# Optimization experiments

Hardware: AMD Instinct MI355X
Metric: run time of the kernel (lower is better)

Reference implementation:

```python
import jax, jax.numpy as jnp
import numpy as np

N_NODES = 5
B, C, H, W = 4, 256, 32, 32
THRESH = 0.3
EPS = 1e-12


def setup_inputs() -> dict:
    key = jax.random.key(0)
    k1, k2, k3, k4 = jax.random.split(key, 4)
    x = jax.random.normal(k1, (N_NODES, B, C, H, W), dtype=jnp.float32)
    w = jax.random.normal(k2, (N_NODES, N_NODES), dtype=jnp.float32)
    # 5 stacked conv1x1 'experts': Conv2d(2C -> C, k=1) weight [C,2C] + bias [C]
    conv_w = jax.random.normal(k3, (N_NODES, C, 2 * C), dtype=jnp.float32) * 0.02
    conv_b = jax.random.normal(k4, (N_NODES, C), dtype=jnp.float32) * 0.02
    return {"x": x, "w": w, "conv_w": conv_w, "conv_b": conv_b}


def reference(x, w, conv_w, conv_b):
    # x: [N, B, C, H, W] -- the list of N node feature maps stacked
    N, b, c, h, ww = x.shape
    P = b * c * h * ww  # 'pixels' = total element count of one node tensor

    # conv_i(cat(node_j, node_i + node_j)) splits into W1@node_j + W2@(node_i+node_j) + b_i
    W1 = conv_w[:, :, :c]          # [N, C, C] acts on node_j
    W2 = conv_w[:, :, c:]          # [N, C, C] acts on node_i + node_j
    A = W1 + W2                    # combined weight on node_j

    term_j = jnp.einsum('ick,jbkhw->ijbchw', A, x)    # [N,N,B,C,H,W]
    term_i = jnp.einsum('ick,ibkhw->ibchw', W2, x)    # [N,B,C,H,W]
    target = term_j + term_i[:, None] + conv_b[:, None, None, :, None, None]
    distance = x[None, :] - target                    # distance[i,j] = node_j - conv_i(...)

    # edge_list[:, i, j] = flatten(distance[i, j])  -> [P, N, N]
    edge = distance.reshape(N, N, P).transpose(2, 0, 1)

    # new_edge = edge * w; sigmoid; threshold at 0.3; L2-normalize over dim=2 (j axis)
    e = jax.nn.sigmoid(edge * w)
    e = jnp.where(e > THRESH, e, jnp.zeros_like(e))
    norm = jnp.sqrt(jnp.sum(e * e, axis=2, keepdims=True))
    e = e / jnp.maximum(norm, EPS)

    # node matrix: [P, N] of flattened node features; fuse h[p,i] = sum_j e[p,i,j]*node[p,j]
    node = x.reshape(N, P).T
    hmat = jnp.einsum('pij,pj->pi', e, node)          # [P, N]
    return hmat.T.reshape(N, b, c, h, ww)
```

## Files before the change

### kernel.cpp

```cpp
#include <hip/hip_runtime.h>
#include <cmath>

#define NN  5
#define BB  4
#define CCH 256
#define HWD 1024
#define THRESH_V 0.3f
#define EPS_V 1e-12f

#define CT 32
#define WT 32
#define KC 32
#define APAD 36
#define SPAD 36

#define SMEM_FLOATS 7424

__global__ __launch_bounds__(384, 4)
void fub_main(const float* __restrict__ x, const float* __restrict__ wmat,
              const float* __restrict__ conv_w, const float* __restrict__ conv_b,
              float* __restrict__ out)
{
    __shared__ __align__(16) float smem[SMEM_FLOATS];
    float* Xs  = smem;
    float* As  = smem + 5120;
    float* W2s = smem + 6272;
    float* Es  = smem;

    const int tid  = threadIdx.x;
    const int wv   = tid >> 6;
    const int lane = tid & 63;

    int bid = blockIdx.x;
    const int hwt = bid & 31; bid >>= 5;
    const int b   = bid & 3;  bid >>= 2;
    const int ct  = bid & 7;  bid >>= 3;
    const int i   = bid;

    const int c0  = ct * CT;
    const int hw0 = hwt * WT;

    const int lr = (lane >> 3) << 2;
    const int lc = (lane & 7)  << 2;

    const int jx = (wv < 5) ? wv : i;
    const float* M = (wv == 5) ? W2s : As;
    const float* Mb = M + lr;
    const float* Xb = Xs + jx * (KC * WT) + lc;

    float acc[4][4];
#pragma unroll
    for (int r = 0; r < 4; ++r)
#pragma unroll
        for (int c = 0; c < 4; ++c) acc[r][c] = 0.0f;

    for (int k0 = 0; k0 < CCH; k0 += KC) {
        if (tid < 320) {
#pragma unroll
            for (int it = 0; it < 4; ++it) {
                const int t   = tid + it * 320;
                const int j   = t >> 8;
                const int rem = t & 255;
                const int kk  = rem >> 3;
                const int p4  = (rem & 7) << 2;
                const float4 v = *(const float4*)(
                    x + (size_t)((j * BB + b) * CCH + k0 + kk) * HWD + hw0 + p4);
                *(float4*)(Xs + j * (KC * WT) + kk * WT + p4) = v;
            }
        } else {
            const int u = tid - 320;
#pragma unroll
            for (int it = 0; it < 4; ++it) {
                const int t  = u + (it << 6);
                const int r  = t >> 3;
                const int kq = (t & 7) << 2;
                const float* base =
                    conv_w + (size_t)(i * CCH + c0 + r) * (2 * CCH) + k0 + kq;
                const float4 w1 = *(const float4*)(base);
                const float4 w2 = *(const float4*)(base + CCH);
                As [(kq + 0) * APAD + r] = w1.x + w2.x;
                As [(kq + 1) * APAD + r] = w1.y + w2.y;
                As [(kq + 2) * APAD + r] = w1.z + w2.z;
                As [(kq + 3) * APAD + r] = w1.w + w2.w;
                W2s[(kq + 0) * APAD + r] = w2.x;
                W2s[(kq + 1) * APAD + r] = w2.y;
                W2s[(kq + 2) * APAD + r] = w2.z;
                W2s[(kq + 3) * APAD + r] = w2.w;
            }
        }
        __syncthreads();

#pragma unroll
        for (int kk = 0; kk < KC; ++kk) {
            const float4 a  = *(const float4*)(Mb + kk * APAD);
            const float4 xv = *(const float4*)(Xb + kk * WT);
            const float ar[4] = {a.x, a.y, a.z, a.w};
            const float xc[4] = {xv.x, xv.y, xv.z, xv.w};
#pragma unroll
            for (int r = 0; r < 4; ++r)
#pragma unroll
                for (int c = 0; c < 4; ++c)
                    acc[r][c] = fmaf(ar[r], xc[c], acc[r][c]);
        }
        __syncthreads();
    }

#pragma unroll
    for (int r = 0; r < 4; ++r) {
        *(float4*)(Es + wv * (CT * SPAD) + (lr + r) * SPAD + lc) =
            make_float4(acc[r][0], acc[r][1], acc[r][2], acc[r][3]);
    }
    __syncthreads();

    if (tid < 256) {
        const int row = tid >> 3;
        const int col = (tid & 7) << 2;
        const int c   = c0 + row;
        const float bias = conv_b[i * CCH + c];

        float wrow[NN];
#pragma unroll
        for (int j = 0; j < NN; ++j) wrow[j] = wmat[i * NN + j];

        const float4 T = *(const float4*)(Es + 5 * (CT * SPAD) + row * SPAD + col);
        const float Tv[4] = {T.x, T.y, T.z, T.w};

        float num[4] = {0.f, 0.f, 0.f, 0.f};
        float sq [4] = {0.f, 0.f, 0.f, 0.f};
#pragma unroll
        for (int j = 0; j < NN; ++j) {
            const float4 s  = *(const float4*)(Es + j * (CT * SPAD) + row * SPAD + col);
            const float4 xj = *(const float4*)(
                x + (size_t)((j * BB + b) * CCH + c) * HWD + hw0 + col);
            const float sv[4] = {s.x, s.y, s.z, s.w};
            const float xv[4] = {xj.x, xj.y, xj.z, xj.w};
#pragma unroll
            for (int cc = 0; cc < 4; ++cc) {
                const float target = sv[cc] + Tv[cc] + bias;
                const float dist   = xv[cc] - target;
                const float z      = dist * wrow[j];
                float e = 1.0f / (1.0f + expf(-z));
                e = (e > THRESH_V) ? e : 0.0f;
                sq[cc]  = fmaf(e, e, sq[cc]);
                num[cc] = fmaf(e, xv[cc], num[cc]);
            }
        }
        float res[4];
#pragma unroll
        for (int cc = 0; cc < 4; ++cc)
            res[cc] = num[cc] / fmaxf(sqrtf(sq[cc]), EPS_V);

        *(float4*)(out + (size_t)((i * BB + b) * CCH + c) * HWD + hw0 + col) =
            make_float4(res[0], res[1], res[2], res[3]);
    }
}

extern "C" void kernel_launch(void* const* d_in, const int* in_sizes, int n_in,
                              void* d_out, int out_size, void* d_ws, size_t ws_size,
                              hipStream_t stream) {
    const float* x      = (const float*)d_in[0];
    const float* w      = (const float*)d_in[1];
    const float* conv_w = (const float*)d_in[2];
    const float* conv_b = (const float*)d_in[3];
    float* out = (float*)d_out;

    dim3 grid(5120);
    dim3 block(384);
    fub_main<<<grid, block, 0, stream>>>(x, w, conv_w, conv_b, out);
}
```

Baseline: 361.5 us.

## Give each wave private LDS tiles with register prefetch and wider pixel tiles

Each wave now stages its own X slice and its own combined weight tile in a private LDS region. This removes both block-wide barriers from the K loop, and the next K chunk is prefetched into registers while the current one is computed. The pixel tile grows to 64 with 8x4 accumulators per thread, halving the grid, and the epilogue uses __expf. In exchange, weight loads are repeated by every wave, LDS use per block rises sharply, which may cut resident blocks, and register pressure grows.

```diff
diff --git a/kernel.cpp b/kernel.cpp
--- a/kernel.cpp
+++ b/kernel.cpp
@@ -9,12 +9,13 @@
 #define EPS_V 1e-12f
 
 #define CT 32
-#define WT 32
-#define KC 32
+#define WT 64
+#define KC 16
 #define APAD 36
-#define SPAD 36
+#define NCHUNK (CCH / KC)
 
-#define SMEM_FLOATS 7424
+#define ESP 68
+#define SMEM_FLOATS 13056
 
 __global__ __launch_bounds__(384, 4)
 void fub_main(const float* __restrict__ x, const float* __restrict__ wmat,
@@ -22,17 +23,13 @@
               float* __restrict__ out)
 {
     __shared__ __align__(16) float smem[SMEM_FLOATS];
-    float* Xs  = smem;
-    float* As  = smem + 5120;
-    float* W2s = smem + 6272;
-    float* Es  = smem;
 
     const int tid  = threadIdx.x;
     const int wv   = tid >> 6;
     const int lane = tid & 63;
 
     int bid = blockIdx.x;
-    const int hwt = bid & 31; bid >>= 5;
+    const int hwt = bid & 15; bid >>= 4;
     const int b   = bid & 3;  bid >>= 2;
     const int ct  = bid & 7;  bid >>= 3;
     const int i   = bid;
@@ -40,118 +37,136 @@
     const int c0  = ct * CT;
     const int hw0 = hwt * WT;
 
-    const int lr = (lane >> 3) << 2;
-    const int lc = (lane & 7)  << 2;
+    float* Xw = smem + wv * (KC * WT);
+    float* Aw = smem + 6144 + wv * (KC * APAD);
+
+    const int lr = (lane >> 4) << 3;
+    const int lc = (lane & 15) << 2;
 
     const int jx = (wv < 5) ? wv : i;
-    const float* M = (wv == 5) ? W2s : As;
-    const float* Mb = M + lr;
-    const float* Xb = Xs + jx * (KC * WT) + lc;
 
-    float acc[4][4];
+    const float* xg = x + (size_t)((jx * BB + b) * CCH) * HWD + hw0;
+    const int xk  = lane >> 4;
+    const int xc4 = (lane & 15) << 2;
+    const int acr = lane >> 1;
+    const int akq = (lane & 1) << 3;
+    const float* wg = conv_w + (size_t)(i * CCH + c0 + acr) * (2 * CCH) + akq;
+
+    float acc[8][4];
 #pragma unroll
-    for (int r = 0; r < 4; ++r)
+    for (int r = 0; r < 8; ++r)
 #pragma unroll
         for (int c = 0; c < 4; ++c) acc[r][c] = 0.0f;
 
-    for (int k0 = 0; k0 < CCH; k0 += KC) {
-        if (tid < 320) {
-#pragma unroll
-            for (int it = 0; it < 4; ++it) {
-                const int t   = tid + it * 320;
-                const int j   = t >> 8;
-                const int rem = t & 255;
-                const int kk  = rem >> 3;
-                const int p4  = (rem & 7) << 2;
-                const float4 v = *(const float4*)(
-                    x + (size_t)((j * BB + b) * CCH + k0 + kk) * HWD + hw0 + p4);
-                *(float4*)(Xs + j * (KC * WT) + kk * WT + p4) = v;
-            }
-        } else {
-            const int u = tid - 320;
-#pragma unroll
-            for (int it = 0; it < 4; ++it) {
-                const int t  = u + (it << 6);
-                const int r  = t >> 3;
-                const int kq = (t & 7) << 2;
-                const float* base =
-                    conv_w + (size_t)(i * CCH + c0 + r) * (2 * CCH) + k0 + kq;
-                const float4 w1 = *(const float4*)(base);
-                const float4 w2 = *(const float4*)(base + CCH);
-                As [(kq + 0) * APAD + r] = w1.x + w2.x;
-                As [(kq + 1) * APAD + r] = w1.y + w2.y;
-                As [(kq + 2) * APAD + r] = w1.z + w2.z;
-                As [(kq + 3) * APAD + r] = w1.w + w2.w;
-                W2s[(kq + 0) * APAD + r] = w2.x;
-                W2s[(kq + 1) * APAD + r] = w2.y;
-                W2s[(kq + 2) * APAD + r] = w2.z;
-                W2s[(kq + 3) * APAD + r] = w2.w;
-            }
-        }
-        __syncthreads();
+    float4 xr[4];
+    float4 w1a, w1b, w2a, w2b;
 
 #pragma unroll
-        for (int kk = 0; kk < KC; ++kk) {
-            const float4 a  = *(const float4*)(Mb + kk * APAD);
-            const float4 xv = *(const float4*)(Xb + kk * WT);
-            const float ar[4] = {a.x, a.y, a.z, a.w};
+    for (int it = 0; it < 4; ++it)
+        xr[it] = *(const float4*)(xg + (size_t)(xk + it * 4) * HWD + xc4);
+    w1a = *(const float4*)(wg);
+    w1b = *(const float4*)(wg + 4);
+    w2a = *(const float4*)(wg + CCH);
+    w2b = *(const float4*)(wg + CCH + 4);
+
+    for (int ch = 0; ch < NCHUNK; ++ch) {
+#pragma unroll
+        for (int it = 0; it < 4; ++it)
+            *(float4*)(Xw + (xk + it * 4) * WT + xc4) = xr[it];
+
+        float av[8];
+        if (wv != 5) {
+            av[0] = w1a.x + w2a.x; av[1] = w1a.y + w2a.y;
+            av[2] = w1a.z + w2a.z; av[3] = w1a.w + w2a.w;
+            av[4] = w1b.x + w2b.x; av[5] = w1b.y + w2b.y;
+            av[6] = w1b.z + w2b.z; av[7] = w1b.w + w2b.w;
+        } else {
+            av[0] = w2a.x; av[1] = w2a.y; av[2] = w2a.z; av[3] = w2a.w;
+            av[4] = w2b.x; av[5] = w2b.y; av[6] = w2b.z; av[7] = w2b.w;
+        }
+#pragma unroll
+        for (int t = 0; t < 8; ++t)
+            Aw[(akq + t) * APAD + acr] = av[t];
+
+        if (ch + 1 < NCHUNK) {
+            const int k0n = (ch + 1) * KC;
+#pragma unroll
+            for (int it = 0; it < 4; ++it)
+                xr[it] = *(const float4*)(xg + (size_t)(k0n + xk + it * 4) * HWD + xc4);
+            const float* wgn = wg + k0n;
+            w1a = *(const float4*)(wgn);
+            w1b = *(const float4*)(wgn + 4);
+            w2a = *(const float4*)(wgn + CCH);
+            w2b = *(const float4*)(wgn + CCH + 4);
+        }
+
+#pragma unroll
+        for (int k = 0; k < KC; ++k) {
+            const float4 a0 = *(const float4*)(Aw + k * APAD + lr);
+            const float4 a1 = *(const float4*)(Aw + k * APAD + lr + 4);
+            const float4 xv = *(const float4*)(Xw + k * WT + lc);
+            const float ar[8] = {a0.x, a0.y, a0.z, a0.w, a1.x, a1.y, a1.z, a1.w};
             const float xc[4] = {xv.x, xv.y, xv.z, xv.w};
 #pragma unroll
-            for (int r = 0; r < 4; ++r)
+            for (int r = 0; r < 8; ++r)
 #pragma unroll
                 for (int c = 0; c < 4; ++c)
                     acc[r][c] = fmaf(ar[r], xc[c], acc[r][c]);
         }
-        __syncthreads();
     }
 
+    __syncthreads();
+    float* Es = smem;
 #pragma unroll
-    for (int r = 0; r < 4; ++r) {
-        *(float4*)(Es + wv * (CT * SPAD) + (lr + r) * SPAD + lc) =
+    for (int r = 0; r < 8; ++r)
+        *(float4*)(Es + wv * (CT * ESP) + (lr + r) * ESP + lc) =
             make_float4(acc[r][0], acc[r][1], acc[r][2], acc[r][3]);
-    }
     __syncthreads();
 
     if (tid < 256) {
-        const int row = tid >> 3;
-        const int col = (tid & 7) << 2;
-        const int c   = c0 + row;
+        const int row  = tid >> 3;
+        const int col8 = (tid & 7) << 3;
+        const int c    = c0 + row;
         const float bias = conv_b[i * CCH + c];
 
         float wrow[NN];
 #pragma unroll
         for (int j = 0; j < NN; ++j) wrow[j] = wmat[i * NN + j];
 
-        const float4 T = *(const float4*)(Es + 5 * (CT * SPAD) + row * SPAD + col);
-        const float Tv[4] = {T.x, T.y, T.z, T.w};
+        const float4 T0 = *(const float4*)(Es + 5 * (CT * ESP) + row * ESP + col8);
+        const float4 T1 = *(const float4*)(Es + 5 * (CT * ESP) + row * ESP + col8 + 4);
+        const float Tv[8] = {T0.x, T0.y, T0.z, T0.w, T1.x, T1.y, T1.z, T1.w};
 
-        float num[4] = {0.f, 0.f, 0.f, 0.f};
-        float sq [4] = {0.f, 0.f, 0.f, 0.f};
+        float num[8] = {0,0,0,0,0,0,0,0};
+        float sq [8] = {0,0,0,0,0,0,0,0};
 #pragma unroll
         for (int j = 0; j < NN; ++j) {
-            const float4 s  = *(const float4*)(Es + j * (CT * SPAD) + row * SPAD + col);
-            const float4 xj = *(const float4*)(
-                x + (size_t)((j * BB + b) * CCH + c) * HWD + hw0 + col);
-            const float sv[4] = {s.x, s.y, s.z, s.w};
-            const float xv[4] = {xj.x, xj.y, xj.z, xj.w};
+            const float4 s0 = *(const float4*)(Es + j * (CT * ESP) + row * ESP + col8);
+            const float4 s1 = *(const float4*)(Es + j * (CT * ESP) + row * ESP + col8 + 4);
+            const float* xp = x + (size_t)((j * BB + b) * CCH + c) * HWD + hw0 + col8;
+            const float4 xa = *(const float4*)(xp);
+            const float4 xb = *(const float4*)(xp + 4);
+            const float sv[8] = {s0.x, s0.y, s0.z, s0.w, s1.x, s1.y, s1.z, s1.w};
+            const float xv[8] = {xa.x, xa.y, xa.z, xa.w, xb.x, xb.y, xb.z, xb.w};
+            const float wj = wrow[j];
 #pragma unroll
-            for (int cc = 0; cc < 4; ++cc) {
-                const float target = sv[cc] + Tv[cc] + bias;
-                const float dist   = xv[cc] - target;
-                const float z      = dist * wrow[j];
-                float e = 1.0f / (1.0f + expf(-z));
+            for (int cc = 0; cc < 8; ++cc) {
+                const float dist = xv[cc] - (sv[cc] + Tv[cc] + bias);
+                const float z    = dist * wj;
+                float e = 1.0f / (1.0f + __expf(-z));
                 e = (e > THRESH_V) ? e : 0.0f;
                 sq[cc]  = fmaf(e, e, sq[cc]);
                 num[cc] = fmaf(e, xv[cc], num[cc]);
             }
         }
-        float res[4];
+        float res[8];
 #pragma unroll
-        for (int cc = 0; cc < 4; ++cc)
+        for (int cc = 0; cc < 8; ++cc)
             res[cc] = num[cc] / fmaxf(sqrtf(sq[cc]), EPS_V);
 
-        *(float4*)(out + (size_t)((i * BB + b) * CCH + c) * HWD + hw0 + col) =
-            make_float4(res[0], res[1], res[2], res[3]);
+        float* op = out + (size_t)((i * BB + b) * CCH + c) * HWD + hw0 + col8;
+        *(float4*)(op)     = make_float4(res[0], res[1], res[2], res[3]);
+        *(float4*)(op + 4) = make_float4(res[4], res[5], res[6], res[7]);
     }
 }
 
@@ -164,7 +179,7 @@
     const float* conv_b = (const float*)d_in[3];
     float* out = (float*)d_out;
 
-    dim3 grid(5120);
+    dim3 grid(2560);
     dim3 block(384);
     fub_main<<<grid, block, 0, stream>>>(x, w, conv_w, conv_b, out);
 }
```

Result: slower. 634.5 us (+75.5%).
